# Kernel tuning notes

Measured on AMD Instinct MI355X. Metric: run time of the kernel, lower is better.

The kernel has to match this reference:

```python
import jax, jax.numpy as jnp
import numpy as np

MU = 0.25  # commitment weight

def setup_inputs() -> dict:
    key = jax.random.key(0)
    k1, k2 = jax.random.split(key)
    x = jax.random.normal(k1, (32, 4096, 32), dtype=jnp.float32)
    codebook = jax.random.normal(k2, (256, 32), dtype=jnp.float32)
    return {"x": x, "codebook": codebook}

def reference(x, codebook):
    B, T, D = x.shape
    K = codebook.shape[0]
    xf = x.reshape(-1, D)  # [N, D]
    d2 = (jnp.sum(xf * xf, axis=-1, keepdims=True)
          + jnp.sum(codebook * codebook, axis=-1)[None, :]
          - 2.0 * (xf @ codebook.T))
    logits = -d2
    probs = jax.nn.softmax(logits, axis=-1)          # [N, K]
    indices = jnp.argmax(logits, axis=-1)            # [N]
    quants_hard = codebook[indices]                  # gather [N, D]
    commitment = jnp.mean((jax.lax.stop_gradient(quants_hard) - xf) ** 2, axis=-1)
    codebook_loss = jnp.mean((quants_hard - jax.lax.stop_gradient(xf)) ** 2, axis=-1)
    loss = codebook_loss + MU * commitment           # [N]
    quants = jax.lax.stop_gradient(quants_hard - xf) + xf  # straight-through
    return (indices.reshape(B, T),
            probs.reshape(B, T, K),
            quants.reshape(B, T, D),
            loss.reshape(B, T))
```

## Files before the change

### kernel.cpp

```cpp
#include <hip/hip_runtime.h>
#include <math.h>

constexpr int D = 32;
constexpr int K = 256;
constexpr int ROWS_PER_BLOCK = 256;


__global__ __launch_bounds__(256) void vq_kernel(
    const float* __restrict__ x,
    const float* __restrict__ cb,
    float* __restrict__ o_idx,
    float* __restrict__ o_probs,
    float* __restrict__ o_quants,
    float* __restrict__ o_loss)
{
    __shared__ float cn[K];
    __shared__ float pbuf[32][257];

    const int tid = threadIdx.x;
    const int n   = blockIdx.x * ROWS_PER_BLOCK + tid;

    {
        const float4* c4 = reinterpret_cast<const float4*>(cb) + tid * (D / 4);
        float a0 = 0.f, a1 = 0.f, a2 = 0.f, a3 = 0.f;
        #pragma unroll
        for (int i = 0; i < D / 4; ++i) {
            float4 c = c4[i];
            a0 += c.x * c.x; a1 += c.y * c.y; a2 += c.z * c.z; a3 += c.w * c.w;
        }
        cn[tid] = (a0 + a1) + (a2 + a3);
    }

    float xr[D];
    {
        const float4* xv = reinterpret_cast<const float4*>(x) + (size_t)n * (D / 4);
        #pragma unroll
        for (int i = 0; i < D / 4; ++i) {
            float4 v = xv[i];
            xr[4 * i + 0] = v.x; xr[4 * i + 1] = v.y;
            xr[4 * i + 2] = v.z; xr[4 * i + 3] = v.w;
        }
    }
    float xx;
    {
        float a0 = 0.f, a1 = 0.f, a2 = 0.f, a3 = 0.f;
        #pragma unroll
        for (int j = 0; j < D; j += 4) {
            a0 += xr[j] * xr[j];     a1 += xr[j + 1] * xr[j + 1];
            a2 += xr[j + 2] * xr[j + 2]; a3 += xr[j + 3] * xr[j + 3];
        }
        xx = (a0 + a1) + (a2 + a3);
    }
    __syncthreads();

    float m = -INFINITY, s = 0.f;
    int bidx = 0;
    #pragma unroll 2
    for (int k = 0; k < K; ++k) {
        const float* c = cb + k * D;
        float d0 = 0.f, d1 = 0.f, d2 = 0.f, d3 = 0.f;
        #pragma unroll
        for (int j = 0; j < D; j += 4) {
            d0 += xr[j] * c[j];         d1 += xr[j + 1] * c[j + 1];
            d2 += xr[j + 2] * c[j + 2]; d3 += xr[j + 3] * c[j + 3];
        }
        float dot = (d0 + d1) + (d2 + d3);
        float lg  = 2.0f * dot - (xx + cn[k]);
        bool  gt  = lg > m;
        bidx      = gt ? k : bidx;
        float mn  = gt ? lg : m;
        s = s * __expf(m - mn) + __expf(lg - mn);
        m = mn;
    }

    o_idx[n] = (float)bidx;

    {
        const float4* cg = reinterpret_cast<const float4*>(cb) + bidx * (D / 4);
        float4* qv = reinterpret_cast<float4*>(o_quants) + (size_t)n * (D / 4);
        float a0 = 0.f, a1 = 0.f, a2 = 0.f, a3 = 0.f;
        #pragma unroll
        for (int i = 0; i < D / 4; ++i) {
            float4 c = cg[i];
            qv[i] = c;
            float e0 = c.x - xr[4 * i + 0], e1 = c.y - xr[4 * i + 1];
            float e2 = c.z - xr[4 * i + 2], e3 = c.w - xr[4 * i + 3];
            a0 += e0 * e0; a1 += e1 * e1; a2 += e2 * e2; a3 += e3 * e3;
        }
        o_loss[n] = ((a0 + a1) + (a2 + a3)) * (1.25f / (float)D);
    }

    const float rs = 1.0f / s;
    const int rowbase = blockIdx.x * ROWS_PER_BLOCK;
    float4* op = reinterpret_cast<float4*>(o_probs);
    for (int cch = 0; cch < 8; ++cch) {
        #pragma unroll 2
        for (int kl = 0; kl < 32; ++kl) {
            int k = cch * 32 + kl;
            const float* c = cb + k * D;
            float d0 = 0.f, d1 = 0.f, d2 = 0.f, d3 = 0.f;
            #pragma unroll
            for (int j = 0; j < D; j += 4) {
                d0 += xr[j] * c[j];         d1 += xr[j + 1] * c[j + 1];
                d2 += xr[j + 2] * c[j + 2]; d3 += xr[j + 3] * c[j + 3];
            }
            float dot = (d0 + d1) + (d2 + d3);
            float lg  = 2.0f * dot - (xx + cn[k]);
            pbuf[kl][tid] = __expf(lg - m) * rs;
        }
        __syncthreads();
        #pragma unroll
        for (int i = 0; i < 8; ++i) {
            int e   = i * 256 + tid;
            int row = e >> 3;
            int jv  = e & 7;
            float4 v;
            v.x = pbuf[4 * jv + 0][row];
            v.y = pbuf[4 * jv + 1][row];
            v.z = pbuf[4 * jv + 2][row];
            v.w = pbuf[4 * jv + 3][row];
            op[(size_t)(rowbase + row) * (K / 4) + cch * 8 + jv] = v;
        }
        __syncthreads();
    }
}

extern "C" void kernel_launch(void* const* d_in, const int* in_sizes, int n_in,
                              void* d_out, int out_size, void* d_ws, size_t ws_size,
                              hipStream_t stream) {
    const float* x  = (const float*)d_in[0];
    const float* cb = (const float*)d_in[1];
    const int N = in_sizes[0] / D;

    float* out      = (float*)d_out;
    float* o_idx    = out;
    float* o_probs  = o_idx + N;
    float* o_quants = o_probs + (size_t)N * K;
    float* o_loss   = o_quants + (size_t)N * D;

    const int grid = N / ROWS_PER_BLOCK;
    vq_kernel<<<grid, ROWS_PER_BLOCK, 0, stream>>>(x, cb, o_idx, o_probs, o_quants, o_loss);
}
```

Before: 222.5 us.

## Split codebook across wavefronts and keep logits in registers, dropping recompute

Each block now handles 64 rows, and each of its four wavefronts computes logits for a 64-entry slice of the codebook. The logits stay in registers, so the second pass that recomputed distances for the probability output is gone, and max and sum are combined across wavefronts through shared memory. Writing the index, the quants and the loss is split across different wavefronts, and probs are staged per wavefront in LDS for coalesced float4 stores. Holding 64 logits per thread raises register pressure, and x is now loaded redundantly by four wavefronts.

```diff
diff --git a/kernel.cpp b/kernel.cpp
--- a/kernel.cpp
+++ b/kernel.cpp
@@ -1,10 +1,10 @@
 #include <hip/hip_runtime.h>
 #include <math.h>
 
-constexpr int D = 32;
-constexpr int K = 256;
-constexpr int ROWS_PER_BLOCK = 256;
-
+constexpr int D    = 32;
+constexpr int K    = 256;
+constexpr int ROWS = 64;
+constexpr int CPT  = 64;
 
 __global__ __launch_bounds__(256) void vq_kernel(
     const float* __restrict__ x,
@@ -14,11 +14,16 @@
     float* __restrict__ o_quants,
     float* __restrict__ o_loss)
 {
-    __shared__ float cn[K];
-    __shared__ float pbuf[32][257];
+    __shared__ float  cn[K];
+    __shared__ float4 pbuf[4][ROWS][9];
+    __shared__ float  mred[4][ROWS];
+    __shared__ float  sred[4][ROWS];
+    __shared__ int    ired[4][ROWS];
 
     const int tid = threadIdx.x;
-    const int n   = blockIdx.x * ROWS_PER_BLOCK + tid;
+    const int l   = tid & 63;
+    const int wu  = __builtin_amdgcn_readfirstlane(tid >> 6);
+    const int row = blockIdx.x * ROWS + l;
 
     {
         const float4* c4 = reinterpret_cast<const float4*>(cb) + tid * (D / 4);
@@ -33,7 +38,7 @@
 
     float xr[D];
     {
-        const float4* xv = reinterpret_cast<const float4*>(x) + (size_t)n * (D / 4);
+        const float4* xv = reinterpret_cast<const float4*>(x) + (size_t)row * (D / 4);
         #pragma unroll
         for (int i = 0; i < D / 4; ++i) {
             float4 v = xv[i];
@@ -46,82 +51,98 @@
         float a0 = 0.f, a1 = 0.f, a2 = 0.f, a3 = 0.f;
         #pragma unroll
         for (int j = 0; j < D; j += 4) {
-            a0 += xr[j] * xr[j];     a1 += xr[j + 1] * xr[j + 1];
+            a0 += xr[j] * xr[j];         a1 += xr[j + 1] * xr[j + 1];
             a2 += xr[j + 2] * xr[j + 2]; a3 += xr[j + 3] * xr[j + 3];
         }
         xx = (a0 + a1) + (a2 + a3);
     }
     __syncthreads();
 
-    float m = -INFINITY, s = 0.f;
-    int bidx = 0;
-    #pragma unroll 2
-    for (int k = 0; k < K; ++k) {
-        const float* c = cb + k * D;
+    const int kbase = wu * CPT;
+    float lg[CPT];
+    #pragma unroll
+    for (int j = 0; j < CPT; ++j) {
+        const float* c = cb + (kbase + j) * D;
         float d0 = 0.f, d1 = 0.f, d2 = 0.f, d3 = 0.f;
         #pragma unroll
-        for (int j = 0; j < D; j += 4) {
-            d0 += xr[j] * c[j];         d1 += xr[j + 1] * c[j + 1];
-            d2 += xr[j + 2] * c[j + 2]; d3 += xr[j + 3] * c[j + 3];
+        for (int t = 0; t < D; t += 4) {
+            d0 += xr[t] * c[t];         d1 += xr[t + 1] * c[t + 1];
+            d2 += xr[t + 2] * c[t + 2]; d3 += xr[t + 3] * c[t + 3];
         }
         float dot = (d0 + d1) + (d2 + d3);
-        float lg  = 2.0f * dot - (xx + cn[k]);
-        bool  gt  = lg > m;
-        bidx      = gt ? k : bidx;
-        float mn  = gt ? lg : m;
-        s = s * __expf(m - mn) + __expf(lg - mn);
-        m = mn;
+        lg[j] = 2.0f * dot - (xx + cn[kbase + j]);
     }
 
-    o_idx[n] = (float)bidx;
+    float m = lg[0]; int bi = 0;
+    #pragma unroll
+    for (int j = 1; j < CPT; ++j) {
+        bool gt = lg[j] > m;
+        m  = gt ? lg[j] : m;
+        bi = gt ? j : bi;
+    }
+    mred[wu][l] = m;
+    ired[wu][l] = kbase + bi;
+    __syncthreads();
 
-    {
-        const float4* cg = reinterpret_cast<const float4*>(cb) + bidx * (D / 4);
-        float4* qv = reinterpret_cast<float4*>(o_quants) + (size_t)n * (D / 4);
+    float gm = mred[0][l]; int gi = ired[0][l];
+    #pragma unroll
+    for (int ww = 1; ww < 4; ++ww) {
+        float mw = mred[ww][l];
+        bool gt  = mw > gm;
+        gi = gt ? ired[ww][l] : gi;
+        gm = gt ? mw : gm;
+    }
+
+    float s = 0.f;
+    #pragma unroll
+    for (int j = 0; j < CPT; ++j) {
+        float e = __expf(lg[j] - gm);
+        lg[j] = e;
+        s += e;
+    }
+    sred[wu][l] = s;
+    __syncthreads();
+    float gs = (sred[0][l] + sred[1][l]) + (sred[2][l] + sred[3][l]);
+    float rs = 1.0f / gs;
+
+    if (wu == 0) {
+        o_idx[row] = (float)gi;
+    } else if (wu == 1) {
+        const float4* cg = reinterpret_cast<const float4*>(cb) + gi * (D / 4);
+        float4* qv = reinterpret_cast<float4*>(o_quants) + (size_t)row * (D / 4);
+        #pragma unroll
+        for (int i = 0; i < D / 4; ++i) qv[i] = cg[i];
+    } else if (wu == 2) {
+        const float4* cg = reinterpret_cast<const float4*>(cb) + gi * (D / 4);
         float a0 = 0.f, a1 = 0.f, a2 = 0.f, a3 = 0.f;
         #pragma unroll
         for (int i = 0; i < D / 4; ++i) {
             float4 c = cg[i];
-            qv[i] = c;
             float e0 = c.x - xr[4 * i + 0], e1 = c.y - xr[4 * i + 1];
             float e2 = c.z - xr[4 * i + 2], e3 = c.w - xr[4 * i + 3];
             a0 += e0 * e0; a1 += e1 * e1; a2 += e2 * e2; a3 += e3 * e3;
         }
-        o_loss[n] = ((a0 + a1) + (a2 + a3)) * (1.25f / (float)D);
+        o_loss[row] = ((a0 + a1) + (a2 + a3)) * (1.25f / (float)D);
     }
 
-    const float rs = 1.0f / s;
-    const int rowbase = blockIdx.x * ROWS_PER_BLOCK;
     float4* op = reinterpret_cast<float4*>(o_probs);
-    for (int cch = 0; cch < 8; ++cch) {
-        #pragma unroll 2
-        for (int kl = 0; kl < 32; ++kl) {
-            int k = cch * 32 + kl;
-            const float* c = cb + k * D;
-            float d0 = 0.f, d1 = 0.f, d2 = 0.f, d3 = 0.f;
-            #pragma unroll
-            for (int j = 0; j < D; j += 4) {
-                d0 += xr[j] * c[j];         d1 += xr[j + 1] * c[j + 1];
-                d2 += xr[j + 2] * c[j + 2]; d3 += xr[j + 3] * c[j + 3];
-            }
-            float dot = (d0 + d1) + (d2 + d3);
-            float lg  = 2.0f * dot - (xx + cn[k]);
-            pbuf[kl][tid] = __expf(lg - m) * rs;
-        }
-        __syncthreads();
+    const int rowbase = blockIdx.x * ROWS;
+    #pragma unroll
+    for (int h = 0; h < 2; ++h) {
         #pragma unroll
         for (int i = 0; i < 8; ++i) {
-            int e   = i * 256 + tid;
-            int row = e >> 3;
-            int jv  = e & 7;
-            float4 v;
-            v.x = pbuf[4 * jv + 0][row];
-            v.y = pbuf[4 * jv + 1][row];
-            v.z = pbuf[4 * jv + 2][row];
-            v.w = pbuf[4 * jv + 3][row];
-            op[(size_t)(rowbase + row) * (K / 4) + cch * 8 + jv] = v;
+            int j = h * 32 + i * 4;
+            pbuf[wu][l][i] = make_float4(lg[j] * rs, lg[j + 1] * rs,
+                                         lg[j + 2] * rs, lg[j + 3] * rs);
         }
-        __syncthreads();
+        #pragma unroll
+        for (int i = 0; i < 8; ++i) {
+            int e  = i * 64 + l;
+            int r  = e >> 3;
+            int c4 = e & 7;
+            float4 v = pbuf[wu][r][c4];
+            op[(size_t)(rowbase + r) * (K / 4) + wu * 16 + h * 8 + c4] = v;
+        }
     }
 }
 
@@ -138,6 +159,6 @@
     float* o_quants = o_probs + (size_t)N * K;
     float* o_loss   = o_quants + (size_t)N * D;
 
-    const int grid = N / ROWS_PER_BLOCK;
-    vq_kernel<<<grid, ROWS_PER_BLOCK, 0, stream>>>(x, cb, o_idx, o_probs, o_quants, o_loss);
+    const int grid = N / ROWS;
+    vq_kernel<<<grid, 256, 0, stream>>>(x, cb, o_idx, o_probs, o_quants, o_loss);
 }
```

Measured after the change: 290.5 us. 1.31x slower.
